# Performance work log

Hardware: AMD Instinct MI355X
Metric: run time of the kernel (lower is better)

Reference implementation:

```python
import jax, jax.numpy as jnp
import numpy as np

VOCAB, D = 32000, 1024
EPS = 1e-5

def setup_inputs() -> dict:
    key = jax.random.key(0)
    k1, k2, k3, k4 = jax.random.split(key, 4)
    patch_embeddings = jax.random.normal(k1, (16, 256, D), dtype=jnp.float32)
    text_prototypes = jax.random.normal(k2, (VOCAB, D), dtype=jnp.float32) * 0.02
    # nn.Linear(d, d): weight [d, d], bias [d]
    lim = 1.0 / np.sqrt(D)
    W = jax.random.uniform(k3, (D, D), minval=-lim, maxval=lim, dtype=jnp.float32)
    b = jax.random.uniform(k4, (D,), minval=-lim, maxval=lim, dtype=jnp.float32)
    gamma = jnp.ones((D,), dtype=jnp.float32)
    beta = jnp.zeros((D,), dtype=jnp.float32)
    return {"patch_embeddings": patch_embeddings, "text_prototypes": text_prototypes,
            "W": W, "b": b, "gamma": gamma, "beta": beta}

def _layer_norm(x, gamma, beta):
    mu = jnp.mean(x, axis=-1, keepdims=True)
    var = jnp.mean(jnp.square(x - mu), axis=-1, keepdims=True)
    return (x - mu) * jax.lax.rsqrt(var + EPS) * gamma + beta

def reference(patch_embeddings, text_prototypes, W, b, gamma, beta):
    # similarities: [B, P, V]
    sims = jnp.einsum('bpd,vd->bpv', patch_embeddings, text_prototypes)
    attn = jax.nn.softmax(sims, axis=-1)
    reprogrammed = jnp.einsum('bpv,vd->bpd', attn, text_prototypes)
    transformed = jnp.einsum('bpd,ed->bpe', reprogrammed, W) + b
    return _layer_norm(patch_embeddings + transformed, gamma, beta)
```

## Files before the change

kernel.cpp:

```cpp
#include <hip/hip_runtime.h>
#include <hip/hip_bf16.h>
#include <cstdint>
#include <cstddef>

#define D_DIM 1024
#define VOCAB 32000
#define ROWS  4096

typedef __attribute__((ext_vector_type(8))) short bf16x8;
typedef __attribute__((ext_vector_type(4))) float f32x4;
typedef __attribute__((ext_vector_type(4))) int   i32x4;
typedef __attribute__((ext_vector_type(8))) int   i32x8;

static __device__ __forceinline__ i32x8 cat8(i32x4 lo, i32x4 hi) {
  return __builtin_shufflevector(lo, hi, 0, 1, 2, 3, 4, 5, 6, 7);
}

static __device__ __forceinline__ unsigned short f2bf(float f) {
  union { float f; unsigned int u; } c; c.f = f;
  unsigned int u = c.u;
  u += 0x7fffu + ((u >> 16) & 1u);
  return (unsigned short)(u >> 16);
}

static __device__ __forceinline__ int pk8(float a, float b) {
  return __builtin_amdgcn_cvt_pk_fp8_f32(a, b, 0, false);
}

static __device__ __forceinline__ void gload_lds16(const void* g, void* s) {
  __builtin_amdgcn_global_load_lds(
      (const __attribute__((address_space(1))) uint32_t*)(g),
      (__attribute__((address_space(3))) uint32_t*)(s), 16, 0, 0);
}

__global__ void k_cvt(const float* __restrict__ src, short* __restrict__ dst, int n4) {
  int i = blockIdx.x * 256 + threadIdx.x;
  if (i < n4) {
    float4 v = *(const float4*)(src + (size_t)i * 4);
    ushort4 u;
    u.x = f2bf(v.x); u.y = f2bf(v.y); u.z = f2bf(v.z); u.w = f2bf(v.w);
    *(ushort4*)(dst + (size_t)i * 4) = u;
  }
}

__global__ void k_cvt_q8(const float* __restrict__ src, uint8_t* __restrict__ dst) {
  int i = blockIdx.x * 256 + threadIdx.x;
  float4 a = *(const float4*)(src + (size_t)i * 8);
  float4 b = *(const float4*)(src + (size_t)i * 8 + 4);
  uint2 o;
  o.x = (pk8(a.x, a.y) & 0xffff) | (pk8(a.z, a.w) << 16);
  o.y = (pk8(b.x, b.y) & 0xffff) | (pk8(b.z, b.w) << 16);
  *(uint2*)(dst + (size_t)i * 8) = o;
}

__global__ void k_prep_K8(const float* __restrict__ src, uint8_t* __restrict__ kb,
                          uint8_t* __restrict__ kt, int R, int C) {
  __shared__ uint8_t tile[64][68];
  int t  = threadIdx.x;
  int r0 = blockIdx.x * 64;
  int c0 = blockIdx.y * 64;
  int lr = t >> 4;
  int lc = (t & 15) * 4;
#pragma unroll
  for (int i = 0; i < 4; ++i) {
    int r = lr + 16 * i;
    float4 v = *(const float4*)(src + (size_t)(r0 + r) * C + c0 + lc);
    unsigned p = (pk8(v.x * 64.f, v.y * 64.f) & 0xffff) | (pk8(v.z * 64.f, v.w * 64.f) << 16);
    *(unsigned*)&tile[r][lc] = p;
    *(unsigned*)(kb + (size_t)(r0 + r) * C + c0 + lc) = p;
  }
  __syncthreads();
#pragma unroll
  for (int i = 0; i < 4; ++i) {
    int c = lr + 16 * i;
    unsigned p = tile[lc + 0][c] | (tile[lc + 1][c] << 8) |
                 (tile[lc + 2][c] << 16) | ((unsigned)tile[lc + 3][c] << 24);
    *(unsigned*)(kt + (size_t)(c0 + c) * R + r0 + lc) = p;
  }
}

#define PS1 416
#define G1NT 8
__global__ __launch_bounds__(512)
__attribute__((amdgpu_waves_per_eu(2)))
void k_g1(
    const uint8_t* __restrict__ A,
    const uint8_t* __restrict__ B,
    uint8_t* __restrict__ Pout, float* __restrict__ den)
{
  __shared__ uint8_t smem[131072];

  int tid  = threadIdx.x;
  int wave = tid >> 6;
  int lane = tid & 63;
  int quad = lane >> 4;
  int t16  = lane & 15;
  int wm = wave >> 1;
  int wn = wave & 1;

  int x  = blockIdx.x & 7;
  int i_ = blockIdx.x >> 3;
  int nt = i_ >> 1;
  int mt = x * 2 + (i_ & 1);
  long mBase = (long)mt * 256;
  long nBase = (long)nt * 256;

  const uint8_t* Ab = A + (size_t)mBase * D_DIM;
  const uint8_t* Bb = B + (size_t)nBase * D_DIM;
  int lrow = lane >> 3;
  int lcol = ((lane & 7) ^ lrow) * 16;

  f32x4 acc[4][8];
#pragma unroll
  for (int i = 0; i < 4; ++i)
#pragma unroll
    for (int j = 0; j < 8; ++j) acc[i][j] = (f32x4){0.f, 0.f, 0.f, 0.f};

  int sw  = t16 & 7;
  int co0 = (((quad << 1) ^ sw) << 4);
  const int SC1 = 0x7F7F7F7F;

  auto STAGE = [&](int slot, int t) {
    uint8_t* As = &smem[slot * 65536];
    uint8_t* Bs = As + 32768;
    int kk = t * 128;
#pragma unroll
    for (int g = 0; g < 4; ++g) {
      int r0 = wave * 32 + g * 8;
      gload_lds16(Ab + (size_t)(r0 + lrow) * D_DIM + kk + lcol, As + r0 * 128);
    }
#pragma unroll
    for (int g = 0; g < 4; ++g) {
      int r0 = wave * 32 + g * 8;
      gload_lds16(Bb + (size_t)(r0 + lrow) * D_DIM + kk + lcol, Bs + r0 * 128);
    }
  };

  STAGE(0, 0);
  STAGE(1, 1);

  for (int t = 0; t < G1NT; ++t) {
    if (t + 1 < G1NT)
      asm volatile("s_waitcnt vmcnt(8)\n\ts_barrier" ::: "memory");
    else
      asm volatile("s_waitcnt vmcnt(0)\n\ts_barrier" ::: "memory");

    const uint8_t* As = &smem[(t & 1) * 65536];
    const uint8_t* Bs = As + 32768;

    i32x8 am[4];
#pragma unroll
    for (int mi = 0; mi < 4; ++mi) {
      const uint8_t* rp = &As[(wm * 64 + mi * 16 + t16) * 128];
      am[mi] = cat8(*(const i32x4*)(rp + co0), *(const i32x4*)(rp + (co0 ^ 16)));
    }
    __builtin_amdgcn_s_setprio(1);
#pragma unroll
    for (int ni = 0; ni < 8; ++ni) {
      const uint8_t* rp = &Bs[(wn * 128 + ni * 16 + t16) * 128];
      i32x8 bfr = cat8(*(const i32x4*)(rp + co0), *(const i32x4*)(rp + (co0 ^ 16)));
#pragma unroll
      for (int mi = 0; mi < 4; ++mi)
        acc[mi][ni] = __builtin_amdgcn_mfma_scale_f32_16x16x128_f8f6f4(
            am[mi], bfr, acc[mi][ni], 0, 0, 0, SC1, 0, SC1);
    }
    __builtin_amdgcn_s_setprio(0);
    asm volatile("s_barrier" ::: "memory");
    if (t + 2 < G1NT) STAGE(t & 1, t + 2);
  }

  float rsum[4][4];
#pragma unroll
  for (int mi = 0; mi < 4; ++mi)
#pragma unroll
    for (int r = 0; r < 4; ++r) rsum[mi][r] = 0.f;
#pragma unroll
  for (int mi = 0; mi < 4; ++mi) {
    int rloc = wm * 64 + mi * 16 + quad * 4;
#pragma unroll
    for (int ni = 0; ni < 8; ++ni) {
      int cloc = wn * 128 + ni * 16 + t16;
#pragma unroll
      for (int r = 0; r < 4; ++r) {
        float e = __expf(acc[mi][ni][r] * 0.015625f);
        smem[(rloc + r) * PS1 + cloc] = (uint8_t)pk8(e, e);
        rsum[mi][r] += e;
      }
    }
  }
#pragma unroll
  for (int mi = 0; mi < 4; ++mi)
#pragma unroll
    for (int r = 0; r < 4; ++r) {
      float s = rsum[mi][r];
      s += __shfl_xor(s, 1);
      s += __shfl_xor(s, 2);
      s += __shfl_xor(s, 4);
      s += __shfl_xor(s, 8);
      if (t16 == 0)
        atomicAdd(&den[mBase + wm * 64 + mi * 16 + quad * 4 + r], s);
    }
  __syncthreads();
  int rr  = tid >> 4;
  int c16 = (tid & 15) * 16;
#pragma unroll
  for (int i = 0; i < 8; ++i) {
    int row = i * 32 + rr;
    i32x4 v = *(const i32x4*)&smem[row * PS1 + c16];
    __builtin_nontemporal_store(v, (i32x4*)&Pout[(size_t)(mBase + row) * VOCAB + nBase + c16]);
  }
}

__global__ __launch_bounds__(512)
__attribute__((amdgpu_waves_per_eu(2)))
void k_g2(
    const uint8_t* __restrict__ P, const uint8_t* __restrict__ KT,
    float* __restrict__ s0, float* __restrict__ s1, float* __restrict__ s2)
{
  __shared__ uint8_t smem[131072];

  int tid  = threadIdx.x;
  int wave = tid >> 6;
  int lane = tid & 63;
  int quad = lane >> 4;
  int t16  = lane & 15;
  int wm = wave >> 1;
  int wn = wave & 1;

  int bid = blockIdx.x;
  int x   = bid & 7;
  int g   = bid >> 3;
  int dt  = x & 3;
  int zz  = (x >> 2) * 2 + (g >> 4);
  int mt  = g & 15;
  long mBase = (long)mt * 256;
  long dBase = (long)dt * 256;
  int  nsteps = (zz < 2) ? 63 : 62;
  long k0 = ((long)zz * 62 + (zz < 2 ? zz : 2)) * 128;

  const uint8_t* Ab = P  + (size_t)mBase * VOCAB + k0;
  const uint8_t* Bb = KT + (size_t)dBase * VOCAB + k0;
  int lrow = lane >> 3;
  int lcol = ((lane & 7) ^ lrow) * 16;

  f32x4 acc[4][8];
#pragma unroll
  for (int i = 0; i < 4; ++i)
#pragma unroll
    for (int j = 0; j < 8; ++j) acc[i][j] = (f32x4){0.f, 0.f, 0.f, 0.f};

  int sw  = t16 & 7;
  int co0 = (((quad << 1) ^ sw) << 4);
  const int SC1 = 0x7F7F7F7F;

  auto STAGE = [&](int slot, int t) {
    uint8_t* As = &smem[slot * 65536];
    uint8_t* Bs = As + 32768;
    long kk = (long)t * 128;
#pragma unroll
    for (int gi = 0; gi < 4; ++gi) {
      int r0 = wave * 32 + gi * 8;
      gload_lds16(Ab + (size_t)(r0 + lrow) * VOCAB + kk + lcol, As + r0 * 128);
    }
#pragma unroll
    for (int gi = 0; gi < 4; ++gi) {
      int r0 = wave * 32 + gi * 8;
      gload_lds16(Bb + (size_t)(r0 + lrow) * VOCAB + kk + lcol, Bs + r0 * 128);
    }
  };

  STAGE(0, 0);
  STAGE(1, 1);

  for (int t = 0; t < nsteps; ++t) {
    if (t + 1 < nsteps)
      asm volatile("s_waitcnt vmcnt(8)\n\ts_barrier" ::: "memory");
    else
      asm volatile("s_waitcnt vmcnt(0)\n\ts_barrier" ::: "memory");

    const uint8_t* As = &smem[(t & 1) * 65536];
    const uint8_t* Bs = As + 32768;

    i32x8 am[4];
#pragma unroll
    for (int mi = 0; mi < 4; ++mi) {
      const uint8_t* rp = &As[(wm * 64 + mi * 16 + t16) * 128];
      am[mi] = cat8(*(const i32x4*)(rp + co0), *(const i32x4*)(rp + (co0 ^ 16)));
    }
    __builtin_amdgcn_s_setprio(1);
#pragma unroll
    for (int ni = 0; ni < 8; ++ni) {
      const uint8_t* rp = &Bs[(wn * 128 + ni * 16 + t16) * 128];
      i32x8 bfr = cat8(*(const i32x4*)(rp + co0), *(const i32x4*)(rp + (co0 ^ 16)));
#pragma unroll
      for (int mi = 0; mi < 4; ++mi)
        acc[mi][ni] = __builtin_amdgcn_mfma_scale_f32_16x16x128_f8f6f4(
            am[mi], bfr, acc[mi][ni], 0, 0, 0, SC1, 0, SC1);
    }
    __builtin_amdgcn_s_setprio(0);
    asm volatile("s_barrier" ::: "memory");
    if (t + 2 < nsteps) STAGE(t & 1, t + 2);
  }

  float* outp = (zz == 1) ? s1 : (zz == 3) ? s2 : s0;
  bool plain = (zz == 1) || (zz == 3);
#pragma unroll
  for (int mi = 0; mi < 4; ++mi) {
    long row = mBase + wm * 64 + mi * 16 + quad * 4;
#pragma unroll
    for (int ni = 0; ni < 8; ++ni) {
      long col = dBase + wn * 128 + ni * 16 + t16;
#pragma unroll
      for (int r = 0; r < 4; ++r) {
        float* p = &outp[(size_t)(row + r) * D_DIM + col];
        if (plain) *p = acc[mi][ni][r];
        else       atomicAdd(p, acc[mi][ni][r]);
      }
    }
  }
}

__global__ __launch_bounds__(256) void k_gemm_bf(
    const short* __restrict__ A, int lda,
    const short* __restrict__ B, int ldb, int Kdim,
    const float* __restrict__ bias, const float* __restrict__ resid,
    float* __restrict__ Cout)
{
  __shared__ short smem[16384];
  short* As = smem;
  short* Bs = smem + 8192;

  int tid  = threadIdx.x;
  int wave = tid >> 6;
  int lane = tid & 63;
  int quad = lane >> 4;
  int t16  = lane & 15;
  int wy = wave >> 1, wx = wave & 1;

  long mBase = (long)blockIdx.y * 128;
  long nBase = (long)blockIdx.x * 128;

  const short* Ab = A + (size_t)mBase * lda;
  const short* Bb = B + (size_t)nBase * ldb;
  int lrow = lane >> 3;
  int lcol = ((lane & 7) ^ lrow) * 8;

  f32x4 acc[4][4];
#pragma unroll
  for (int i = 0; i < 4; ++i)
#pragma unroll
    for (int j = 0; j < 4; ++j) acc[i][j] = (f32x4){0.f, 0.f, 0.f, 0.f};

  int sw = t16 & 7;

  for (int kk = 0; kk < Kdim; kk += 64) {
#pragma unroll
    for (int i = 0; i < 4; ++i) {
      int row = wave * 32 + i * 8;
      gload_lds16(Ab + (size_t)(row + lrow) * lda + kk + lcol, &As[row * 64]);
      gload_lds16(Bb + (size_t)(row + lrow) * ldb + kk + lcol, &Bs[row * 64]);
    }
    __syncthreads();
#pragma unroll
    for (int kc = 0; kc < 8; kc += 4) {
      bf16x8 af[4], bfr[4];
#pragma unroll
      for (int mi = 0; mi < 4; ++mi)
        af[mi] = *(const bf16x8*)&As[(wy * 64 + mi * 16 + t16) * 64 +
                                     (((kc + quad) ^ sw) << 3)];
#pragma unroll
      for (int ni = 0; ni < 4; ++ni)
        bfr[ni] = *(const bf16x8*)&Bs[(wx * 64 + ni * 16 + t16) * 64 +
                                      (((kc + quad) ^ sw) << 3)];
#pragma unroll
      for (int mi = 0; mi < 4; ++mi)
#pragma unroll
        for (int ni = 0; ni < 4; ++ni)
          acc[mi][ni] = __builtin_amdgcn_mfma_f32_16x16x32_bf16(af[mi], bfr[ni],
                                                                acc[mi][ni], 0, 0, 0);
    }
    __syncthreads();
  }

#pragma unroll
  for (int mi = 0; mi < 4; ++mi) {
    long row = mBase + wy * 64 + mi * 16 + quad * 4;
#pragma unroll
    for (int ni = 0; ni < 4; ++ni) {
      long col = nBase + wx * 64 + ni * 16 + t16;
#pragma unroll
      for (int r = 0; r < 4; ++r) {
        size_t idx = (size_t)(row + r) * 1024 + col;
        Cout[idx] = acc[mi][ni][r] + bias[col] + resid[idx];
      }
    }
  }
}

__global__ void k_div(const float* __restrict__ s0, const float* __restrict__ s1,
                      const float* __restrict__ s2,
                      const float* __restrict__ den, short* __restrict__ out) {
  int i = (blockIdx.x * 256 + threadIdx.x) * 4;
  float4 a = *(const float4*)(s0 + i);
  float4 b = *(const float4*)(s1 + i);
  float4 c = *(const float4*)(s2 + i);
  float inv = 0.015625f / den[i >> 10];
  ushort4 u;
  u.x = f2bf((a.x + b.x + c.x) * inv); u.y = f2bf((a.y + b.y + c.y) * inv);
  u.z = f2bf((a.z + b.z + c.z) * inv); u.w = f2bf((a.w + b.w + c.w) * inv);
  *(ushort4*)(out + i) = u;
}

__global__ __launch_bounds__(256) void k_ln(const float* __restrict__ x,
                                            const float* __restrict__ gamma,
                                            const float* __restrict__ beta,
                                            float* __restrict__ out) {
  __shared__ float s_sum[4], s_sq[4];
  int row = blockIdx.x;
  int tid = threadIdx.x;
  const float* xr = x + (size_t)row * 1024;
  float4 v = *(const float4*)(xr + tid * 4);
  float s = v.x + v.y + v.z + v.w;
  float q = v.x * v.x + v.y * v.y + v.z * v.z + v.w * v.w;
#pragma unroll
  for (int off = 32; off >= 1; off >>= 1) {
    s += __shfl_down(s, off);
    q += __shfl_down(q, off);
  }
  int wv = tid >> 6;
  if ((tid & 63) == 0) { s_sum[wv] = s; s_sq[wv] = q; }
  __syncthreads();
  float tot  = s_sum[0] + s_sum[1] + s_sum[2] + s_sum[3];
  float totq = s_sq[0] + s_sq[1] + s_sq[2] + s_sq[3];
  float mu   = tot * (1.0f / 1024.0f);
  float var  = totq * (1.0f / 1024.0f) - mu * mu;
  float rstd = rsqrtf(var + 1e-5f);
  float4 g = *(const float4*)(gamma + tid * 4);
  float4 b = *(const float4*)(beta + tid * 4);
  float4 o;
  o.x = (v.x - mu) * rstd * g.x + b.x;
  o.y = (v.y - mu) * rstd * g.y + b.y;
  o.z = (v.z - mu) * rstd * g.z + b.z;
  o.w = (v.w - mu) * rstd * g.w + b.w;
  *(float4*)(out + (size_t)row * 1024 + tid * 4) = o;
}

extern "C" void kernel_launch(void* const* d_in, const int* in_sizes, int n_in,
                              void* d_out, int out_size, void* d_ws, size_t ws_size,
                              hipStream_t stream) {
  const float* patch = (const float*)d_in[0];
  const float* proto = (const float*)d_in[1];
  const float* W     = (const float*)d_in[2];
  const float* bvec  = (const float*)d_in[3];
  const float* gamma = (const float*)d_in[4];
  const float* beta  = (const float*)d_in[5];
  float* out = (float*)d_out;

  char* ws = (char*)d_ws;
  size_t off = 0;
  uint8_t* Q8  = (uint8_t*)(ws + off); off += (size_t)ROWS * D_DIM;
  uint8_t* Kb8 = (uint8_t*)(ws + off); off += (size_t)VOCAB * D_DIM;
  uint8_t* KT8 = (uint8_t*)(ws + off); off += (size_t)VOCAB * D_DIM;
  short*   Wb  = (short*)(ws + off);   off += (size_t)D_DIM * D_DIM * 2;
  short*   Rb  = (short*)(ws + off);   off += (size_t)ROWS * D_DIM * 2;
  uint8_t* P8  = (uint8_t*)(ws + off); off += (size_t)ROWS * VOCAB;
  float*   num = (float*)(ws + off);   off += (size_t)ROWS * D_DIM * 4;
  float*   den = (float*)(ws + off);   off += (size_t)ROWS * 4;
  float*   pre = (float*)P8;
  float*   sz0 = (float*)(ws);
  float*   sz1 = (float*)(ws + (size_t)16 * 1024 * 1024);
  float*   sz2 = num;

  hipMemsetAsync(den, 0, ROWS * sizeof(float), stream);

  k_cvt_q8<<<ROWS * D_DIM / 8 / 256, 256, 0, stream>>>(patch, Q8);
  k_cvt<<<D_DIM * D_DIM / 4 / 256, 256, 0, stream>>>(W, Wb, D_DIM * D_DIM / 4);
  k_prep_K8<<<dim3(VOCAB / 64, D_DIM / 64), 256, 0, stream>>>(proto, Kb8, KT8, VOCAB, D_DIM);

  k_g1<<<2000, 512, 0, stream>>>(Q8, Kb8, P8, den);

  hipMemsetAsync(sz0, 0, (size_t)16 * 1024 * 1024, stream);

  k_g2<<<256, 512, 0, stream>>>(P8, KT8, sz0, sz1, sz2);

  k_div<<<ROWS * D_DIM / 4 / 256, 256, 0, stream>>>(sz0, sz1, sz2, den, Rb);

  k_gemm_bf<<<dim3(D_DIM / 128, ROWS / 128), 256, 0, stream>>>(
      Rb, D_DIM, Wb, D_DIM, D_DIM, bvec, patch, pre);

  k_ln<<<ROWS, 256, 0, stream>>>(pre, gamma, beta, out);
}
```

Measured before the change: 642.9 us.

## Interleave next-tile global loads with MFMA phases and swizzle epilogue LDS layout

New measurement: 642.3 us. Within noise of the previous version (-0.1%).

```diff
diff --git a/kernel.cpp b/kernel.cpp
--- a/kernel.cpp
+++ b/kernel.cpp
@@ -79,7 +79,7 @@
   }
 }
 
-#define PS1 416
+#define PS1 272
 #define G1NT 8
 __global__ __launch_bounds__(512)
 __attribute__((amdgpu_waves_per_eu(2)))
@@ -128,45 +128,57 @@
     for (int g = 0; g < 4; ++g) {
       int r0 = wave * 32 + g * 8;
       gload_lds16(Ab + (size_t)(r0 + lrow) * D_DIM + kk + lcol, As + r0 * 128);
-    }
-#pragma unroll
-    for (int g = 0; g < 4; ++g) {
-      int r0 = wave * 32 + g * 8;
       gload_lds16(Bb + (size_t)(r0 + lrow) * D_DIM + kk + lcol, Bs + r0 * 128);
     }
   };
 
   STAGE(0, 0);
-  STAGE(1, 1);
 
   for (int t = 0; t < G1NT; ++t) {
-    if (t + 1 < G1NT)
-      asm volatile("s_waitcnt vmcnt(8)\n\ts_barrier" ::: "memory");
-    else
-      asm volatile("s_waitcnt vmcnt(0)\n\ts_barrier" ::: "memory");
+    asm volatile("s_waitcnt vmcnt(0)\n\ts_barrier" ::: "memory");
 
     const uint8_t* As = &smem[(t & 1) * 65536];
     const uint8_t* Bs = As + 32768;
+    uint8_t* Asn = &smem[((t + 1) & 1) * 65536];
+    uint8_t* Bsn = Asn + 32768;
+    int kk1 = (t + 1) * 128;
+    bool st = (t + 1 < G1NT);
 
     i32x8 am[4];
 #pragma unroll
-    for (int mi = 0; mi < 4; ++mi) {
-      const uint8_t* rp = &As[(wm * 64 + mi * 16 + t16) * 128];
-      am[mi] = cat8(*(const i32x4*)(rp + co0), *(const i32x4*)(rp + (co0 ^ 16)));
-    }
-    __builtin_amdgcn_s_setprio(1);
-#pragma unroll
-    for (int ni = 0; ni < 8; ++ni) {
-      const uint8_t* rp = &Bs[(wn * 128 + ni * 16 + t16) * 128];
-      i32x8 bfr = cat8(*(const i32x4*)(rp + co0), *(const i32x4*)(rp + (co0 ^ 16)));
+    for (int p = 0; p < 4; ++p) {
+      if (p == 0) {
+#pragma unroll
+        for (int mi = 0; mi < 4; ++mi) {
+          const uint8_t* rp = &As[(wm * 64 + mi * 16 + t16) * 128];
+          am[mi] = cat8(*(const i32x4*)(rp + co0), *(const i32x4*)(rp + (co0 ^ 16)));
+        }
+      }
+      int ni0 = 2 * p;
+      const uint8_t* rp0 = &Bs[(wn * 128 + ni0 * 16 + t16) * 128];
+      i32x8 b0 = cat8(*(const i32x4*)(rp0 + co0), *(const i32x4*)(rp0 + (co0 ^ 16)));
+      const uint8_t* rp1 = &Bs[(wn * 128 + (ni0 + 1) * 16 + t16) * 128];
+      i32x8 b1 = cat8(*(const i32x4*)(rp1 + co0), *(const i32x4*)(rp1 + (co0 ^ 16)));
+      if (st) {
+        int r0 = wave * 32 + p * 8;
+        gload_lds16(Ab + (size_t)(r0 + lrow) * D_DIM + kk1 + lcol, Asn + r0 * 128);
+        gload_lds16(Bb + (size_t)(r0 + lrow) * D_DIM + kk1 + lcol, Bsn + r0 * 128);
+      }
+      asm volatile("s_barrier" ::: "memory");
+      asm volatile("s_waitcnt lgkmcnt(0)" ::: "memory");
+      __builtin_amdgcn_sched_barrier(0);
+      __builtin_amdgcn_s_setprio(1);
 #pragma unroll
       for (int mi = 0; mi < 4; ++mi)
-        acc[mi][ni] = __builtin_amdgcn_mfma_scale_f32_16x16x128_f8f6f4(
-            am[mi], bfr, acc[mi][ni], 0, 0, 0, SC1, 0, SC1);
-    }
-    __builtin_amdgcn_s_setprio(0);
-    asm volatile("s_barrier" ::: "memory");
-    if (t + 2 < G1NT) STAGE(t & 1, t + 2);
+        acc[mi][ni0] = __builtin_amdgcn_mfma_scale_f32_16x16x128_f8f6f4(
+            am[mi], b0, acc[mi][ni0], 0, 0, 0, SC1, 0, SC1);
+#pragma unroll
+      for (int mi = 0; mi < 4; ++mi)
+        acc[mi][ni0 + 1] = __builtin_amdgcn_mfma_scale_f32_16x16x128_f8f6f4(
+            am[mi], b1, acc[mi][ni0 + 1], 0, 0, 0, SC1, 0, SC1);
+      __builtin_amdgcn_s_setprio(0);
+      asm volatile("s_barrier" ::: "memory");
+    }
   }
 
   float rsum[4][4];
@@ -180,10 +192,11 @@
 #pragma unroll
     for (int ni = 0; ni < 8; ++ni) {
       int cloc = wn * 128 + ni * 16 + t16;
+      int csw  = cloc ^ (quad << 4);
 #pragma unroll
       for (int r = 0; r < 4; ++r) {
         float e = __expf(acc[mi][ni][r] * 0.015625f);
-        smem[(rloc + r) * PS1 + cloc] = (uint8_t)pk8(e, e);
+        smem[(rloc + r) * PS1 + csw] = (uint8_t)pk8(e, e);
         rsum[mi][r] += e;
       }
     }
@@ -206,7 +219,8 @@
 #pragma unroll
   for (int i = 0; i < 8; ++i) {
     int row = i * 32 + rr;
-    i32x4 v = *(const i32x4*)&smem[row * PS1 + c16];
+    int q2  = ((row >> 2) & 3) << 4;
+    i32x4 v = *(const i32x4*)&smem[row * PS1 + (c16 ^ q2)];
     __builtin_nontemporal_store(v, (i32x4*)&Pout[(size_t)(mBase + row) * VOCAB + nBase + c16]);
   }
 }
@@ -261,45 +275,57 @@
     for (int gi = 0; gi < 4; ++gi) {
       int r0 = wave * 32 + gi * 8;
       gload_lds16(Ab + (size_t)(r0 + lrow) * VOCAB + kk + lcol, As + r0 * 128);
-    }
-#pragma unroll
-    for (int gi = 0; gi < 4; ++gi) {
-      int r0 = wave * 32 + gi * 8;
       gload_lds16(Bb + (size_t)(r0 + lrow) * VOCAB + kk + lcol, Bs + r0 * 128);
     }
   };
 
   STAGE(0, 0);
-  STAGE(1, 1);
 
   for (int t = 0; t < nsteps; ++t) {
-    if (t + 1 < nsteps)
-      asm volatile("s_waitcnt vmcnt(8)\n\ts_barrier" ::: "memory");
-    else
-      asm volatile("s_waitcnt vmcnt(0)\n\ts_barrier" ::: "memory");
+    asm volatile("s_waitcnt vmcnt(0)\n\ts_barrier" ::: "memory");
 
     const uint8_t* As = &smem[(t & 1) * 65536];
     const uint8_t* Bs = As + 32768;
+    uint8_t* Asn = &smem[((t + 1) & 1) * 65536];
+    uint8_t* Bsn = Asn + 32768;
+    long kk1 = (long)(t + 1) * 128;
+    bool st = (t + 1 < nsteps);
 
     i32x8 am[4];
 #pragma unroll
-    for (int mi = 0; mi < 4; ++mi) {
-      const uint8_t* rp = &As[(wm * 64 + mi * 16 + t16) * 128];
-      am[mi] = cat8(*(const i32x4*)(rp + co0), *(const i32x4*)(rp + (co0 ^ 16)));
-    }
-    __builtin_amdgcn_s_setprio(1);
-#pragma unroll
-    for (int ni = 0; ni < 8; ++ni) {
-      const uint8_t* rp = &Bs[(wn * 128 + ni * 16 + t16) * 128];
-      i32x8 bfr = cat8(*(const i32x4*)(rp + co0), *(const i32x4*)(rp + (co0 ^ 16)));
+    for (int p = 0; p < 4; ++p) {
+      if (p == 0) {
+#pragma unroll
+        for (int mi = 0; mi < 4; ++mi) {
+          const uint8_t* rp = &As[(wm * 64 + mi * 16 + t16) * 128];
+          am[mi] = cat8(*(const i32x4*)(rp + co0), *(const i32x4*)(rp + (co0 ^ 16)));
+        }
+      }
+      int ni0 = 2 * p;
+      const uint8_t* rp0 = &Bs[(wn * 128 + ni0 * 16 + t16) * 128];
+      i32x8 b0 = cat8(*(const i32x4*)(rp0 + co0), *(const i32x4*)(rp0 + (co0 ^ 16)));
+      const uint8_t* rp1 = &Bs[(wn * 128 + (ni0 + 1) * 16 + t16) * 128];
+      i32x8 b1 = cat8(*(const i32x4*)(rp1 + co0), *(const i32x4*)(rp1 + (co0 ^ 16)));
+      if (st) {
+        int r0 = wave * 32 + p * 8;
+        gload_lds16(Ab + (size_t)(r0 + lrow) * VOCAB + kk1 + lcol, Asn + r0 * 128);
+        gload_lds16(Bb + (size_t)(r0 + lrow) * VOCAB + kk1 + lcol, Bsn + r0 * 128);
+      }
+      asm volatile("s_barrier" ::: "memory");
+      asm volatile("s_waitcnt lgkmcnt(0)" ::: "memory");
+      __builtin_amdgcn_sched_barrier(0);
+      __builtin_amdgcn_s_setprio(1);
 #pragma unroll
       for (int mi = 0; mi < 4; ++mi)
-        acc[mi][ni] = __builtin_amdgcn_mfma_scale_f32_16x16x128_f8f6f4(
-            am[mi], bfr, acc[mi][ni], 0, 0, 0, SC1, 0, SC1);
-    }
-    __builtin_amdgcn_s_setprio(0);
-    asm volatile("s_barrier" ::: "memory");
-    if (t + 2 < nsteps) STAGE(t & 1, t + 2);
+        acc[mi][ni0] = __builtin_amdgcn_mfma_scale_f32_16x16x128_f8f6f4(
+            am[mi], b0, acc[mi][ni0], 0, 0, 0, SC1, 0, SC1);
+#pragma unroll
+      for (int mi = 0; mi < 4; ++mi)
+        acc[mi][ni0 + 1] = __builtin_amdgcn_mfma_scale_f32_16x16x128_f8f6f4(
+            am[mi], b1, acc[mi][ni0 + 1], 0, 0, 0, SC1, 0, SC1);
+      __builtin_amdgcn_s_setprio(0);
+      asm volatile("s_barrier" ::: "memory");
+    }
   }
 
   float* outp = (zz == 1) ? s1 : (zz == 3) ? s2 : s0;
```
